# Kernel tuning notes

Hardware: AMD Instinct MI355X
Metric: run time of the kernel (lower is better)

Reference implementation:

```python
import jax, jax.numpy as jnp
import numpy as np

N, T, E = 50000, 12, 800000
IN_DIM, SP_DIM, TP_DIM = 128, 128, 128


def setup_inputs() -> dict:
    key = jax.random.key(0)
    ks = jax.random.split(key, 9)
    h = jax.random.normal(ks[0], (N, T, IN_DIM), dtype=jnp.float32)
    src = jax.random.randint(ks[1], (E,), 0, N, dtype=jnp.int32)
    dst = jax.random.randint(ks[2], (E,), 0, N, dtype=jnp.int32)
    s = 1.0 / np.sqrt(IN_DIM).astype(np.float32)
    # GraphConv layer weights (xavier-ish) and zero biases, layer1: in->sp, layer2: sp->sp
    Wg1 = jax.random.normal(ks[3], (IN_DIM, SP_DIM), dtype=jnp.float32) * s
    bg1 = jnp.zeros((SP_DIM,), jnp.float32)
    Wg2 = jax.random.normal(ks[4], (SP_DIM, SP_DIM), dtype=jnp.float32) * s
    bg2 = jnp.zeros((SP_DIM,), jnp.float32)
    # LSTM params, torch layout: [4H, in]/[4H, H], gate order i,f,g,o
    t = 1.0 / np.sqrt(TP_DIM).astype(np.float32)
    w_ih = jax.random.uniform(ks[5], (4 * TP_DIM, IN_DIM), jnp.float32, -t, t)
    w_hh = jax.random.uniform(ks[6], (4 * TP_DIM, TP_DIM), jnp.float32, -t, t)
    b_ih = jax.random.uniform(ks[7], (4 * TP_DIM,), jnp.float32, -t, t)
    b_hh = jax.random.uniform(ks[8], (4 * TP_DIM,), jnp.float32, -t, t)
    return dict(h=h, src=src, dst=dst, Wg1=Wg1, bg1=bg1, Wg2=Wg2, bg2=bg2,
                w_ih=w_ih, w_hh=w_hh, b_ih=b_ih, b_hh=b_hh)


def _graph_conv(x, src, dst, norm_src, norm_dst, W, b):
    # DGL GraphConv norm='both': D_out^{-1/2} on source feats, sum-aggregate to dst,
    # D_in^{-1/2} on result, then dense weight + bias.
    x = x * norm_src                                  # [N, D]
    m = jax.ops.segment_sum(x[src], dst, num_segments=N)  # SpMM: [N, D]
    m = m * norm_dst
    return m @ W + b


def reference(h, src, dst, Wg1, bg1, Wg2, bg2, w_ih, w_hh, b_ih, b_hh):
    ones_e = jnp.ones((E,), jnp.float32)
    out_deg = jnp.maximum(jax.ops.segment_sum(ones_e, src, num_segments=N), 1.0)
    in_deg = jnp.maximum(jax.ops.segment_sum(ones_e, dst, num_segments=N), 1.0)
    norm_src = (out_deg ** -0.5)[:, None]
    norm_dst = (in_deg ** -0.5)[:, None]

    hs_list = []
    for i in range(T):  # fixed small time horizon
        x = h[:, i]  # [N, IN_DIM]
        x = jax.nn.gelu(_graph_conv(x, src, dst, norm_src, norm_dst, Wg1, bg1), approximate=False)
        x = jax.nn.gelu(_graph_conv(x, src, dst, norm_src, norm_dst, Wg2, bg2), approximate=False)
        hs_list.append(jnp.mean(x, axis=0))  # dgl.mean_nodes over the single graph
    hs = jnp.stack(hs_list, axis=0)[None]  # [1, T, SP_DIM]

    # temporal branch: LSTM over time, nodes as batch, then mean over time
    def lstm_step(carry, x_t):
        hp, cp = carry
        gates = x_t @ w_ih.T + b_ih + hp @ w_hh.T + b_hh  # [N, 4H]
        i_, f_, g_, o_ = jnp.split(gates, 4, axis=-1)
        c = jax.nn.sigmoid(f_) * cp + jax.nn.sigmoid(i_) * jnp.tanh(g_)
        ho = jax.nn.sigmoid(o_) * jnp.tanh(c)
        return (ho, c), ho

    h0 = jnp.zeros((N, TP_DIM), jnp.float32)
    _, ht_seq = jax.lax.scan(lstm_step, (h0, h0), jnp.swapaxes(h, 0, 1))  # [T, N, H]
    ht = jnp.mean(ht_seq, axis=0)  # torch.mean over dim=1 (time) -> [N, H]
    return hs, ht
```

## Files before the change

### kernel.cpp

```cpp
#include <hip/hip_runtime.h>
#include <math.h>

#define NN 50000
#define TT 12
#define EE 800000
#define DIM 128

typedef short bf16x8 __attribute__((ext_vector_type(8)));
typedef float f32x4 __attribute__((ext_vector_type(4)));

__device__ __forceinline__ float sigmoidf_(float x) { return 1.0f / (1.0f + expf(-x)); }
__device__ __forceinline__ float geluf_(float x) {
  return 0.5f * x * (1.0f + erff(x * 0.70710678118654752440f));
}
#define LOG2E 1.44269504088896340736f
__device__ __forceinline__ float fsigmoid(float x) {
  return __builtin_amdgcn_rcpf(1.0f + __builtin_amdgcn_exp2f(-LOG2E * x));
}
__device__ __forceinline__ float ftanh(float x) {
  return 1.0f - 2.0f * __builtin_amdgcn_rcpf(1.0f + __builtin_amdgcn_exp2f((2.0f * LOG2E) * x));
}
__device__ __forceinline__ unsigned short f2b(float f) {
  union { float f; unsigned u; } v;
  v.f = f;
  unsigned r = (v.u + 0x7fffu + ((v.u >> 16) & 1u)) >> 16;
  return (unsigned short)r;
}
__device__ __forceinline__ float blo(unsigned u) {
  union { unsigned x; float f; } v; v.x = u << 16; return v.f;
}
__device__ __forceinline__ float bhi(unsigned u) {
  union { unsigned x; float f; } v; v.x = u & 0xffff0000u; return v.f;
}
__device__ __forceinline__ float b2f(unsigned short b) {
  union { unsigned u; float f; } v; v.u = ((unsigned)b) << 16; return v.f;
}
__device__ __forceinline__ unsigned short f2h(float f) {
  union { _Float16 h; unsigned short s; } v; v.h = (_Float16)f; return v.s;
}
__device__ __forceinline__ float h2f(unsigned short u) {
  union { unsigned short s; _Float16 h; } v; v.s = u; return (float)v.h;
}


__global__ void deg_kernel(const int* __restrict__ src, const int* __restrict__ dst,
                           int* __restrict__ ds, int* __restrict__ dd) {
  int e = blockIdx.x * 256 + threadIdx.x;
  if (e < EE) {
    atomicAdd(&ds[src[e]], 1);
    atomicAdd(&dd[dst[e]], 1);
  }
}

__global__ void norm_kernel(const int* __restrict__ ds, const int* __restrict__ dd,
                            float* __restrict__ ns, float* __restrict__ nd) {
  int i = blockIdx.x * 256 + threadIdx.x;
  if (i < NN) {
    ns[i] = rsqrtf((float)(ds[i] > 1 ? ds[i] : 1));
    nd[i] = rsqrtf((float)(dd[i] > 1 ? dd[i] : 1));
  }
}

__global__ void scan_kernel(const int* __restrict__ cnt, int* __restrict__ row_ptr, int n) {
  __shared__ int sm[1024];
  __shared__ int carry;
  int tid = threadIdx.x;
  if (tid == 0) carry = 0;
  __syncthreads();
  for (int base = 0; base < n; base += 1024) {
    int v = (base + tid < n) ? cnt[base + tid] : 0;
    sm[tid] = v;
    __syncthreads();
    for (int off = 1; off < 1024; off <<= 1) {
      int t = (tid >= off) ? sm[tid - off] : 0;
      __syncthreads();
      sm[tid] += t;
      __syncthreads();
    }
    int incl = sm[tid];
    if (base + tid < n) row_ptr[base + tid] = carry + incl - v;
    int tot = sm[1023];
    __syncthreads();
    if (tid == 0) carry += tot;
    __syncthreads();
  }
  if (tid == 0) row_ptr[n] = carry;
}

__global__ void csr_kernel(const int* __restrict__ src, const int* __restrict__ dst,
                           const int* __restrict__ row_ptr, int* __restrict__ fill,
                           int* __restrict__ col) {
  int e = blockIdx.x * 256 + threadIdx.x;
  if (e < EE) {
    int d = dst[e];
    int pos = row_ptr[d] + atomicAdd(&fill[d], 1);
    col[pos] = src[e];
  }
}


__global__ void prep_w(const float* __restrict__ Wg1, const float* __restrict__ Wg2,
                       const float* __restrict__ wih, const float* __restrict__ whh,
                       const float* __restrict__ bih, const float* __restrict__ bhh,
                       unsigned short* __restrict__ W2bt, unsigned short* __restrict__ Wcomb,
                       unsigned short* __restrict__ whhb, float* __restrict__ bgate) {
  int i = blockIdx.x * 256 + threadIdx.x;
  if (i < 16384) {
    int n = i >> 7, k = i & 127;
    W2bt[i] = f2b(Wg2[k * 128 + n]);
  }
  int j = i - 16384;
  if (j >= 0 && j < 81920) {
    int n = j >> 7, k = j & 127;
    Wcomb[j] = f2b(n < 128 ? Wg1[k * 128 + n] : wih[(n - 128) * 128 + k]);
  }
  int q = i - (16384 + 81920);
  if (q >= 0 && q < 65536) whhb[q] = f2b(whh[q]);
  if (i < 512) bgate[i] = bih[i] + bhh[i];
}

#define LDT 40

__global__ __launch_bounds__(256) void gemm_h_all(
    const float* __restrict__ A, const float* __restrict__ ns,
    const unsigned short* __restrict__ Wcomb, unsigned short* __restrict__ C,
    unsigned short* __restrict__ xg, int M) {
  __shared__ unsigned short As[4 * 128 * LDT];
  __shared__ unsigned short Bs[128 * LDT];
  const int tid = threadIdx.x;
  const int lane = tid & 63, wid = tid >> 6;
  const int quad = lane >> 4, l16 = lane & 15;
  const int row0 = blockIdx.x * 128;
  const int wm = (wid >> 1) * 64, wn = (wid & 1) * 64;

#pragma unroll
  for (int rds = 0; rds < 8; rds++) {
    int idx = rds * 256 + tid;
    int m = idx >> 4;
    int k8 = (idx & 15) * 8;
    int gr = row0 + m;
    if (gr >= M) gr = M - 1;
    const float4 va = *(const float4*)(A + (size_t)gr * 128 + k8);
    const float4 vb = *(const float4*)(A + (size_t)gr * 128 + k8 + 4);
    int chunk = k8 >> 5, c = k8 & 31;
    unsigned short* d = &As[(chunk * 128 + m) * LDT + c];
    d[0] = f2b(va.x); d[1] = f2b(va.y); d[2] = f2b(va.z); d[3] = f2b(va.w);
    d[4] = f2b(vb.x); d[5] = f2b(vb.y); d[6] = f2b(vb.z); d[7] = f2b(vb.w);
  }

  for (int cb = 0; cb < 5; cb++) {
    f32x4 acc[4][4] = {};
#pragma unroll
    for (int k0 = 0; k0 < 4; k0++) {
      __syncthreads();
      {
        int n = tid >> 1;
        int c = (tid & 1) * 16;
        const unsigned short* srcw = Wcomb + ((size_t)(cb * 128 + n)) * 128 + k0 * 32 + c;
        *(uint4*)(&Bs[n * LDT + c]) = *(const uint4*)srcw;
        *(uint4*)(&Bs[n * LDT + c + 8]) = *(const uint4*)(srcw + 8);
      }
      __syncthreads();
      bf16x8 af[4], bfr[4];
#pragma unroll
      for (int im = 0; im < 4; im++)
        af[im] = *(const bf16x8*)(&As[(k0 * 128 + wm + im * 16 + l16) * LDT + quad * 8]);
#pragma unroll
      for (int in = 0; in < 4; in++)
        bfr[in] = *(const bf16x8*)(&Bs[(wn + in * 16 + l16) * LDT + quad * 8]);
#pragma unroll
      for (int im = 0; im < 4; im++)
#pragma unroll
        for (int in = 0; in < 4; in++)
          acc[im][in] = __builtin_amdgcn_mfma_f32_16x16x32_bf16(af[im], bfr[in], acc[im][in], 0, 0, 0);
    }
    if (cb == 0) {
#pragma unroll
      for (int im = 0; im < 4; im++)
#pragma unroll
        for (int r = 0; r < 4; r++) {
          int row = row0 + wm + im * 16 + quad * 4 + r;
          if (row < M) {
            float s = ns[row / TT];
#pragma unroll
            for (int in = 0; in < 4; in++)
              C[(size_t)row * 128 + wn + in * 16 + l16] = f2b(acc[im][in][r] * s);
          }
        }
    } else {
      const int goff = (cb - 1) * 128;
#pragma unroll
      for (int im = 0; im < 4; im++)
#pragma unroll
        for (int r = 0; r < 4; r++) {
          int row = row0 + wm + im * 16 + quad * 4 + r;
          if (row < M)
#pragma unroll
            for (int in = 0; in < 4; in++)
              xg[(size_t)row * 512 + goff + wn + in * 16 + l16] = f2h(acc[im][in][r]);
        }
    }
  }
}

__global__ __launch_bounds__(256) void gemm_bf16A(
    const unsigned short* __restrict__ A, const unsigned short* __restrict__ Bt,
    unsigned short* __restrict__ C, int M) {
  __shared__ unsigned short As[128 * LDT];
  __shared__ unsigned short Bs[128 * LDT];
  const int tid = threadIdx.x;
  const int lane = tid & 63, wid = tid >> 6;
  const int quad = lane >> 4, l16 = lane & 15;
  const int row0 = blockIdx.x * 128;
  const int wm = (wid >> 1) * 64, wn = (wid & 1) * 64;
  f32x4 acc[4][4] = {};
  for (int k0 = 0; k0 < 128; k0 += 32) {
#pragma unroll
    for (int rds = 0; rds < 2; rds++) {
      int idx = (rds * 256 + tid) * 8;
      int m = idx >> 5, c = idx & 31;
      int gr = row0 + m;
      if (gr >= M) gr = M - 1;
      *(uint4*)(&As[m * LDT + c]) = *(const uint4*)(A + (size_t)gr * 128 + k0 + c);
      *(uint4*)(&Bs[m * LDT + c]) = *(const uint4*)(Bt + m * 128 + k0 + c);
    }
    __syncthreads();
    bf16x8 af[4], bfr[4];
#pragma unroll
    for (int im = 0; im < 4; im++)
      af[im] = *(const bf16x8*)(&As[(wm + im * 16 + l16) * LDT + quad * 8]);
#pragma unroll
    for (int in = 0; in < 4; in++)
      bfr[in] = *(const bf16x8*)(&Bs[(wn + in * 16 + l16) * LDT + quad * 8]);
#pragma unroll
    for (int im = 0; im < 4; im++)
#pragma unroll
      for (int in = 0; in < 4; in++)
        acc[im][in] = __builtin_amdgcn_mfma_f32_16x16x32_bf16(af[im], bfr[in], acc[im][in], 0, 0, 0);
    __syncthreads();
  }
#pragma unroll
  for (int im = 0; im < 4; im++)
#pragma unroll
    for (int r = 0; r < 4; r++) {
      int row = row0 + wm + im * 16 + quad * 4 + r;
      if (row < M)
#pragma unroll
        for (int in = 0; in < 4; in++)
          C[(size_t)row * 128 + wn + in * 16 + l16] = f2b(acc[im][in][r]);
    }
}


template <bool SCALE_OUT>
__global__ __launch_bounds__(256) void spmm_b(
    const unsigned short* __restrict__ z, const int* __restrict__ rowp,
    const int* __restrict__ colx, const float* __restrict__ ns,
    const float* __restrict__ nd, const float* __restrict__ bg,
    unsigned short* __restrict__ y) {
  int d = (blockIdx.x * 256 + threadIdx.x) >> 6;
  int lane = threadIdx.x & 63;
  if (d >= NN) return;
  int beg = rowp[d], end = rowp[d + 1];
  float acc[3][8] = {};
  int j = beg;
  int s = (j < end) ? colx[j] : 0;
  while (j < end) {
    int snext = (j + 1 < end) ? colx[j + 1] : 0;
    const unsigned short* base = z + (size_t)s * 1536 + lane * 8;
#pragma unroll
    for (int r = 0; r < 3; r++) {
      uint4 v = *(const uint4*)(base + r * 512);
      acc[r][0] += blo(v.x); acc[r][1] += bhi(v.x);
      acc[r][2] += blo(v.y); acc[r][3] += bhi(v.y);
      acc[r][4] += blo(v.z); acc[r][5] += bhi(v.z);
      acc[r][6] += blo(v.w); acc[r][7] += bhi(v.w);
    }
    s = snext;
    j++;
  }
  float scn = nd[d];
  float sco = SCALE_OUT ? ns[d] : 1.0f;
  float bgv[8];
#pragma unroll
  for (int k = 0; k < 8; k++) bgv[k] = bg[(lane * 8 + k) & 127];
  unsigned short* outp = y + (size_t)d * 1536 + lane * 8;
#pragma unroll
  for (int r = 0; r < 3; r++) {
    unsigned short o[8];
#pragma unroll
    for (int k = 0; k < 8; k++)
      o[k] = f2b(sco * geluf_(acc[r][k] * scn + bgv[k]));
    *(uint4*)(outp + r * 512) = *(const uint4*)o;
  }
}


__global__ void colmean_b(const unsigned short* __restrict__ x, float* __restrict__ out) {
  int t = blockIdx.x;
  int cc = threadIdx.x & 127;
  int half = threadIdx.x >> 7;
  float s = 0.f;
  for (int n = blockIdx.y * 2 + half; n < NN; n += 64)
    s += b2f(x[((size_t)n * TT + t) * 128 + cc]);
  __shared__ float sm[256];
  sm[threadIdx.x] = s;
  __syncthreads();
  if (threadIdx.x < 128)
    atomicAdd(&out[t * 128 + cc], (sm[threadIdx.x] + sm[threadIdx.x + 128]) * (1.0f / NN));
}

#define HPLD 136

__global__ __launch_bounds__(512, 2) void lstm_hh(
    const unsigned short* __restrict__ whhb, const unsigned short* __restrict__ xg,
    const float* __restrict__ bgate, float* __restrict__ ht_out, int M) {
  __shared__ unsigned short Hp[64 * HPLD];
  const int tid = threadIdx.x;
  const int lane = tid & 63;
  const int w = tid >> 6;
  const int quad = lane >> 4, l16 = lane & 15;
  const int row0 = blockIdx.x * 64;
  const int colg = w * 16 + l16;

  bf16x8 bw[4][4];
#pragma unroll
  for (int g = 0; g < 4; g++)
#pragma unroll
    for (int k0 = 0; k0 < 4; k0++)
      bw[g][k0] = *(const bf16x8*)(whhb + ((size_t)(g * 128 + colg)) * 128 + k0 * 32 + quad * 8);

  float cs[4][4], hacc[4][4];
#pragma unroll
  for (int im = 0; im < 4; im++)
#pragma unroll
    for (int r = 0; r < 4; r++) { cs[im][r] = 0.f; hacc[im][r] = 0.f; }

  const float bi = bgate[colg], bff = bgate[128 + colg];
  const float bgg = bgate[256 + colg], bo = bgate[384 + colg];

  for (int t = 0; t < TT; t++) {
    f32x4 acc[4][4] = {};
    if (t) {
#pragma unroll
      for (int k0 = 0; k0 < 4; k0++) {
        bf16x8 af[4];
#pragma unroll
        for (int im = 0; im < 4; im++)
          af[im] = *(const bf16x8*)(&Hp[(im * 16 + l16) * HPLD + k0 * 32 + quad * 8]);
#pragma unroll
        for (int g = 0; g < 4; g++)
#pragma unroll
          for (int im = 0; im < 4; im++)
            acc[im][g] = __builtin_amdgcn_mfma_f32_16x16x32_bf16(af[im], bw[g][k0], acc[im][g], 0, 0, 0);
      }
    }

    unsigned short xsv[4][4][4];
#pragma unroll
    for (int im = 0; im < 4; im++)
#pragma unroll
      for (int r = 0; r < 4; r++) {
        int gr = row0 + im * 16 + quad * 4 + r;
        int grc = gr < M ? gr : M - 1;
        const unsigned short* xp = xg + ((size_t)grc * TT + t) * 512 + colg;
#pragma unroll
        for (int g = 0; g < 4; g++) xsv[im][r][g] = xp[g * 128];
      }

    if (t) __syncthreads();

#pragma unroll
    for (int im = 0; im < 4; im++)
#pragma unroll
      for (int r = 0; r < 4; r++) {
        float iv = fsigmoid(acc[im][0][r] + h2f(xsv[im][r][0]) + bi);
        float fv = fsigmoid(acc[im][1][r] + h2f(xsv[im][r][1]) + bff);
        float gv = ftanh(acc[im][2][r] + h2f(xsv[im][r][2]) + bgg);
        float ov = fsigmoid(acc[im][3][r] + h2f(xsv[im][r][3]) + bo);
        float cn = fv * cs[im][r] + iv * gv;
        cs[im][r] = cn;
        float ho = ov * ftanh(cn);
        hacc[im][r] += ho;
        Hp[(im * 16 + quad * 4 + r) * HPLD + colg] = f2b(ho);
      }
    __syncthreads();
  }
#pragma unroll
  for (int im = 0; im < 4; im++)
#pragma unroll
    for (int r = 0; r < 4; r++) {
      int gr = row0 + im * 16 + quad * 4 + r;
      if (gr < M) ht_out[(size_t)gr * 128 + colg] = hacc[im][r] * (1.0f / TT);
    }
}


extern "C" void kernel_launch(void* const* d_in, const int* in_sizes, int n_in,
                              void* d_out, int out_size, void* d_ws, size_t ws_size,
                              hipStream_t stream) {
  const float* h   = (const float*)d_in[0];
  const int*   src = (const int*)d_in[1];
  const int*   dst = (const int*)d_in[2];
  const float* Wg1 = (const float*)d_in[3];
  const float* bg1 = (const float*)d_in[4];
  const float* Wg2 = (const float*)d_in[5];
  const float* bg2 = (const float*)d_in[6];
  const float* wih = (const float*)d_in[7];
  const float* whh = (const float*)d_in[8];
  const float* bih = (const float*)d_in[9];
  const float* bhh = (const float*)d_in[10];

  float* out = (float*)d_out;
  float* hs_out = out;
  float* ht_out = out + TT * DIM;

  char* p = (char*)d_ws;
  auto alloc = [&](size_t bytes) -> void* {
    void* r = (void*)p;
    p += (bytes + 255) & ~(size_t)255;
    return r;
  };
  const size_t MB = (size_t)NN * TT * DIM;
  unsigned short* bufA = (unsigned short*)alloc(MB * 2);
  unsigned short* bufB = (unsigned short*)alloc(MB * 2);
  unsigned short* xgb  = (unsigned short*)alloc((size_t)NN * TT * 512 * 2);
  unsigned short* W2bt = (unsigned short*)alloc(16384 * 2);
  unsigned short* Wcomb= (unsigned short*)alloc(81920 * 2);
  unsigned short* whhb = (unsigned short*)alloc(65536 * 2);
  float* bgate = (float*)alloc(512 * 4);
  float* ns    = (float*)alloc(NN * 4);
  float* nd    = (float*)alloc(NN * 4);
  int* degs    = (int*)alloc(NN * 4);
  int* degd    = (int*)alloc(NN * 4);
  int* rowp    = (int*)alloc((NN + 1) * 4);
  int* colx    = (int*)alloc(EE * 4);

  hipMemsetAsync(degs, 0, NN * 4, stream);
  hipMemsetAsync(degd, 0, NN * 4, stream);
  hipMemsetAsync(hs_out, 0, TT * DIM * 4, stream);

  deg_kernel<<<(EE + 255) / 256, 256, 0, stream>>>(src, dst, degs, degd);
  norm_kernel<<<(NN + 255) / 256, 256, 0, stream>>>(degs, degd, ns, nd);
  scan_kernel<<<1, 1024, 0, stream>>>(degd, rowp, NN);
  hipMemsetAsync(degs, 0, NN * 4, stream);
  csr_kernel<<<(EE + 255) / 256, 256, 0, stream>>>(src, dst, rowp, degs, colx);
  prep_w<<<(16384 + 81920 + 65536 + 255) / 256, 256, 0, stream>>>(
      Wg1, Wg2, wih, whh, bih, bhh, W2bt, Wcomb, whhb, bgate);

  const int M = NN * TT;
  const int gblocks = (M + 127) / 128;
  const int sblocks = (NN + 3) / 4;

  gemm_h_all<<<gblocks, 256, 0, stream>>>(h, ns, Wcomb, bufA, xgb, M);
  spmm_b<true><<<sblocks, 256, 0, stream>>>(bufA, rowp, colx, ns, nd, bg1, bufB);
  gemm_bf16A<<<gblocks, 256, 0, stream>>>(bufB, W2bt, bufA, M);
  spmm_b<false><<<sblocks, 256, 0, stream>>>(bufA, rowp, colx, ns, nd, bg2, bufB);
  colmean_b<<<dim3(TT, 32), 256, 0, stream>>>(bufB, hs_out);

  lstm_hh<<<(NN + 63) / 64, 512, 0, stream>>>(whhb, xgb, bgate, ht_out, NN);
}
```

Measured before the change: 2.313 ms.

## Interleave LSTM gate preactivations per column and prefetch next timestep

The input-gate GEMM now packs the four fp16 gate values for each column into one 8-byte word, so the xg layout becomes column-interleaved and is written with uint2 stores instead of scattered 2-byte stores. The LSTM recurrence kernel reads each row's four gates with a single uint2 load and double-buffers those loads, fetching timestep t+1 while step t's MFMA and gate math run. Launch bounds drop to one block per CU so the extra registers fit. The cost is higher register pressure in both kernels and possibly lower occupancy.

```diff
diff --git a/kernel.cpp b/kernel.cpp
--- a/kernel.cpp
+++ b/kernel.cpp
@@ -148,6 +148,10 @@
     d[4] = f2b(vb.x); d[5] = f2b(vb.y); d[6] = f2b(vb.z); d[7] = f2b(vb.w);
   }
 
+  unsigned ps01[4][4][4];
+  unsigned ps23[4][4][4];
+
+#pragma unroll
   for (int cb = 0; cb < 5; cb++) {
     f32x4 acc[4][4] = {};
 #pragma unroll
@@ -188,19 +192,36 @@
           }
         }
     } else {
-      const int goff = (cb - 1) * 128;
 #pragma unroll
       for (int im = 0; im < 4; im++)
 #pragma unroll
-        for (int r = 0; r < 4; r++) {
-          int row = row0 + wm + im * 16 + quad * 4 + r;
-          if (row < M)
-#pragma unroll
-            for (int in = 0; in < 4; in++)
-              xg[(size_t)row * 512 + goff + wn + in * 16 + l16] = f2h(acc[im][in][r]);
+        for (int in = 0; in < 4; in++)
+#pragma unroll
+          for (int r = 0; r < 4; r++) {
+            unsigned u = (unsigned)f2h(acc[im][in][r]);
+            if (cb == 1) ps01[im][in][r] = u;
+            else if (cb == 2) ps01[im][in][r] |= u << 16;
+            else if (cb == 3) ps23[im][in][r] = u;
+            else ps23[im][in][r] |= u << 16;
+          }
+    }
+  }
+
+#pragma unroll
+  for (int im = 0; im < 4; im++)
+#pragma unroll
+    for (int r = 0; r < 4; r++) {
+      int row = row0 + wm + im * 16 + quad * 4 + r;
+      if (row < M) {
+#pragma unroll
+        for (int in = 0; in < 4; in++) {
+          uint2 v;
+          v.x = ps01[im][in][r];
+          v.y = ps23[im][in][r];
+          *(uint2*)(xg + (size_t)row * 512 + (size_t)(wn + in * 16 + l16) * 4) = v;
         }
-    }
-  }
+      }
+    }
 }
 
 __global__ __launch_bounds__(256) void gemm_bf16A(
@@ -312,7 +333,56 @@
 
 #define HPLD 136
 
-__global__ __launch_bounds__(512, 2) void lstm_hh(
+#define XLOAD(XN, TQ)                                                          \
+  {                                                                            \
+    _Pragma("unroll") for (int im = 0; im < 4; im++) {                         \
+      _Pragma("unroll") for (int r = 0; r < 4; r++) {                          \
+        int gr = row0 + im * 16 + quad * 4 + r;                                \
+        int grc = gr < M ? gr : M - 1;                                         \
+        XN[im][r] = *(const uint2*)(xg + ((size_t)grc * TT + (TQ)) * 512 +     \
+                                    (size_t)colg * 4);                         \
+      }                                                                        \
+    }                                                                          \
+  }
+
+#define LSTEP(T, XC, XN)                                                       \
+  {                                                                            \
+    f32x4 acc[4][4] = {};                                                      \
+    if ((T) > 0) {                                                             \
+      _Pragma("unroll") for (int k0 = 0; k0 < 4; k0++) {                       \
+        bf16x8 af[4];                                                          \
+        _Pragma("unroll") for (int im = 0; im < 4; im++) {                     \
+          af[im] = *(const bf16x8*)(&Hp[(im * 16 + l16) * HPLD + k0 * 32 +     \
+                                        quad * 8]);                            \
+        }                                                                      \
+        _Pragma("unroll") for (int g = 0; g < 4; g++) {                        \
+          _Pragma("unroll") for (int im = 0; im < 4; im++) {                   \
+            acc[im][g] = __builtin_amdgcn_mfma_f32_16x16x32_bf16(              \
+                af[im], bw[g][k0], acc[im][g], 0, 0, 0);                       \
+          }                                                                    \
+        }                                                                      \
+      }                                                                        \
+    }                                                                          \
+    if ((T) + 1 < TT) XLOAD(XN, (T) + 1)                                       \
+    if ((T) > 0) __syncthreads();                                              \
+    _Pragma("unroll") for (int im = 0; im < 4; im++) {                         \
+      _Pragma("unroll") for (int r = 0; r < 4; r++) {                          \
+        uint2 xv = XC[im][r];                                                  \
+        float iv = fsigmoid(acc[im][0][r] + h2f((unsigned short)(xv.x & 0xffffu)) + bi);  \
+        float fv = fsigmoid(acc[im][1][r] + h2f((unsigned short)(xv.x >> 16)) + bff);     \
+        float gv = ftanh(acc[im][2][r] + h2f((unsigned short)(xv.y & 0xffffu)) + bgg);    \
+        float ov = fsigmoid(acc[im][3][r] + h2f((unsigned short)(xv.y >> 16)) + bo);      \
+        float cn = fv * cs[im][r] + iv * gv;                                   \
+        cs[im][r] = cn;                                                        \
+        float ho = ov * ftanh(cn);                                             \
+        hacc[im][r] += ho;                                                     \
+        Hp[(im * 16 + quad * 4 + r) * HPLD + colg] = f2b(ho);                  \
+      }                                                                        \
+    }                                                                          \
+    __syncthreads();                                                           \
+  }
+
+__global__ __launch_bounds__(512, 1) void lstm_hh(
     const unsigned short* __restrict__ whhb, const unsigned short* __restrict__ xg,
     const float* __restrict__ bgate, float* __restrict__ ht_out, int M) {
   __shared__ unsigned short Hp[64 * HPLD];
@@ -339,53 +409,15 @@
   const float bi = bgate[colg], bff = bgate[128 + colg];
   const float bgg = bgate[256 + colg], bo = bgate[384 + colg];
 
-  for (int t = 0; t < TT; t++) {
-    f32x4 acc[4][4] = {};
-    if (t) {
-#pragma unroll
-      for (int k0 = 0; k0 < 4; k0++) {
-        bf16x8 af[4];
-#pragma unroll
-        for (int im = 0; im < 4; im++)
-          af[im] = *(const bf16x8*)(&Hp[(im * 16 + l16) * HPLD + k0 * 32 + quad * 8]);
-#pragma unroll
-        for (int g = 0; g < 4; g++)
-#pragma unroll
-          for (int im = 0; im < 4; im++)
-            acc[im][g] = __builtin_amdgcn_mfma_f32_16x16x32_bf16(af[im], bw[g][k0], acc[im][g], 0, 0, 0);
-      }
-    }
-
-    unsigned short xsv[4][4][4];
-#pragma unroll
-    for (int im = 0; im < 4; im++)
-#pragma unroll
-      for (int r = 0; r < 4; r++) {
-        int gr = row0 + im * 16 + quad * 4 + r;
-        int grc = gr < M ? gr : M - 1;
-        const unsigned short* xp = xg + ((size_t)grc * TT + t) * 512 + colg;
-#pragma unroll
-        for (int g = 0; g < 4; g++) xsv[im][r][g] = xp[g * 128];
-      }
-
-    if (t) __syncthreads();
-
-#pragma unroll
-    for (int im = 0; im < 4; im++)
-#pragma unroll
-      for (int r = 0; r < 4; r++) {
-        float iv = fsigmoid(acc[im][0][r] + h2f(xsv[im][r][0]) + bi);
-        float fv = fsigmoid(acc[im][1][r] + h2f(xsv[im][r][1]) + bff);
-        float gv = ftanh(acc[im][2][r] + h2f(xsv[im][r][2]) + bgg);
-        float ov = fsigmoid(acc[im][3][r] + h2f(xsv[im][r][3]) + bo);
-        float cn = fv * cs[im][r] + iv * gv;
-        cs[im][r] = cn;
-        float ho = ov * ftanh(cn);
-        hacc[im][r] += ho;
-        Hp[(im * 16 + quad * 4 + r) * HPLD + colg] = f2b(ho);
-      }
-    __syncthreads();
-  }
+  uint2 xA[4][4], xB[4][4];
+  XLOAD(xA, 0)
+
+#pragma unroll
+  for (int tt = 0; tt < TT; tt += 2) {
+    LSTEP(tt, xA, xB)
+    LSTEP(tt + 1, xB, xA)
+  }
+
 #pragma unroll
   for (int im = 0; im < 4; im++)
 #pragma unroll
```

Result: slower. 2.707 ms (+17.0%).

## Interleave LSTM input-gate precomputation per column for vectorized loads

Applied to the files above, without the earlier changes.

The input-projection GEMM now packs the four gate values for each hidden column into one 8-byte word, so xg is laid out column-major over gates instead of gate-blocked. The LSTM recurrence kernel then loads all four gates with a single uint2 load per row, issued at the top of each timestep before the MFMA work so the load latency overlaps compute. Launch bounds drop to one block per SM-equivalent to allow more registers, and the time loop is kept rolled. The GEMM epilogue must hold all gate results in registers across the cb loop, which raises register pressure there.

```diff
diff --git a/kernel.cpp b/kernel.cpp
--- a/kernel.cpp
+++ b/kernel.cpp
@@ -148,6 +148,10 @@
     d[4] = f2b(vb.x); d[5] = f2b(vb.y); d[6] = f2b(vb.z); d[7] = f2b(vb.w);
   }
 
+  unsigned ps01[4][4][4];
+  unsigned ps23[4][4][4];
+
+#pragma unroll
   for (int cb = 0; cb < 5; cb++) {
     f32x4 acc[4][4] = {};
 #pragma unroll
@@ -188,19 +192,36 @@
           }
         }
     } else {
-      const int goff = (cb - 1) * 128;
 #pragma unroll
       for (int im = 0; im < 4; im++)
 #pragma unroll
-        for (int r = 0; r < 4; r++) {
-          int row = row0 + wm + im * 16 + quad * 4 + r;
-          if (row < M)
-#pragma unroll
-            for (int in = 0; in < 4; in++)
-              xg[(size_t)row * 512 + goff + wn + in * 16 + l16] = f2h(acc[im][in][r]);
+        for (int in = 0; in < 4; in++)
+#pragma unroll
+          for (int r = 0; r < 4; r++) {
+            unsigned u = (unsigned)f2h(acc[im][in][r]);
+            if (cb == 1) ps01[im][in][r] = u;
+            else if (cb == 2) ps01[im][in][r] |= u << 16;
+            else if (cb == 3) ps23[im][in][r] = u;
+            else ps23[im][in][r] |= u << 16;
+          }
+    }
+  }
+
+#pragma unroll
+  for (int im = 0; im < 4; im++)
+#pragma unroll
+    for (int r = 0; r < 4; r++) {
+      int row = row0 + wm + im * 16 + quad * 4 + r;
+      if (row < M) {
+#pragma unroll
+        for (int in = 0; in < 4; in++) {
+          uint2 v;
+          v.x = ps01[im][in][r];
+          v.y = ps23[im][in][r];
+          *(uint2*)(xg + (size_t)row * 512 + (size_t)(wn + in * 16 + l16) * 4) = v;
         }
-    }
-  }
+      }
+    }
 }
 
 __global__ __launch_bounds__(256) void gemm_bf16A(
@@ -312,7 +333,7 @@
 
 #define HPLD 136
 
-__global__ __launch_bounds__(512, 2) void lstm_hh(
+__global__ __launch_bounds__(512, 1) void lstm_hh(
     const unsigned short* __restrict__ whhb, const unsigned short* __restrict__ xg,
     const float* __restrict__ bgate, float* __restrict__ ht_out, int M) {
   __shared__ unsigned short Hp[64 * HPLD];
@@ -339,7 +360,18 @@
   const float bi = bgate[colg], bff = bgate[128 + colg];
   const float bgg = bgate[256 + colg], bo = bgate[384 + colg];
 
+#pragma unroll 1
   for (int t = 0; t < TT; t++) {
+    uint2 xv[4][4];
+#pragma unroll
+    for (int im = 0; im < 4; im++)
+#pragma unroll
+      for (int r = 0; r < 4; r++) {
+        int gr = row0 + im * 16 + quad * 4 + r;
+        int grc = gr < M ? gr : M - 1;
+        xv[im][r] = *(const uint2*)(xg + ((size_t)grc * TT + t) * 512 + (size_t)colg * 4);
+      }
+
     f32x4 acc[4][4] = {};
     if (t) {
 #pragma unroll
@@ -354,30 +386,18 @@
           for (int im = 0; im < 4; im++)
             acc[im][g] = __builtin_amdgcn_mfma_f32_16x16x32_bf16(af[im], bw[g][k0], acc[im][g], 0, 0, 0);
       }
-    }
-
-    unsigned short xsv[4][4][4];
+      __syncthreads();
+    }
+
 #pragma unroll
     for (int im = 0; im < 4; im++)
 #pragma unroll
       for (int r = 0; r < 4; r++) {
-        int gr = row0 + im * 16 + quad * 4 + r;
-        int grc = gr < M ? gr : M - 1;
-        const unsigned short* xp = xg + ((size_t)grc * TT + t) * 512 + colg;
-#pragma unroll
-        for (int g = 0; g < 4; g++) xsv[im][r][g] = xp[g * 128];
-      }
-
-    if (t) __syncthreads();
-
-#pragma unroll
-    for (int im = 0; im < 4; im++)
-#pragma unroll
-      for (int r = 0; r < 4; r++) {
-        float iv = fsigmoid(acc[im][0][r] + h2f(xsv[im][r][0]) + bi);
-        float fv = fsigmoid(acc[im][1][r] + h2f(xsv[im][r][1]) + bff);
-        float gv = ftanh(acc[im][2][r] + h2f(xsv[im][r][2]) + bgg);
-        float ov = fsigmoid(acc[im][3][r] + h2f(xsv[im][r][3]) + bo);
+        uint2 xvv = xv[im][r];
+        float iv = fsigmoid(acc[im][0][r] + h2f((unsigned short)(xvv.x & 0xffffu)) + bi);
+        float fv = fsigmoid(acc[im][1][r] + h2f((unsigned short)(xvv.x >> 16)) + bff);
+        float gv = ftanh(acc[im][2][r] + h2f((unsigned short)(xvv.y & 0xffffu)) + bgg);
+        float ov = fsigmoid(acc[im][3][r] + h2f((unsigned short)(xvv.y >> 16)) + bo);
         float cn = fv * cs[im][r] + iv * gv;
         cs[im][r] = cn;
         float ho = ov * ftanh(cn);
```

Result: slower. 2.467 ms (+6.7%).
